# Performance work log

Hardware: AMD Instinct MI355X
Metric: run time of the kernel (lower is better)

## Reference

```python
import jax, jax.numpy as jnp
import numpy as np

N_NODES = 50000
IN_FEATS, HID_FEATS, OUT_FEATS, HEADS = 128, 32, 64, 4
NEG_SLOPE = 0.2
EPS = 1e-16


def gat_conv(x, src, dst, W, att_src, att_dst, bias, heads, out_ch, concat):
    """PyG-style GATConv. src/dst: [E] (self-loops already included).
    W: [in, heads*out_ch]; att_src/att_dst: [heads, out_ch]; bias: [heads*out_ch] or [out_ch].
    """
    n = x.shape[0]
    xw = (x @ W).reshape(n, heads, out_ch)                     # [N,H,C]
    a_src = (xw * att_src).sum(-1)                             # [N,H]
    a_dst = (xw * att_dst).sum(-1)                             # [N,H]
    e = jax.nn.leaky_relu(a_src[src] + a_dst[dst], NEG_SLOPE)  # [E,H]
    # segment softmax over incoming edges of each destination node
    m = jax.ops.segment_max(e, dst, num_segments=n)
    e = jnp.exp(e - m[dst])
    denom = jax.ops.segment_sum(e, dst, num_segments=n)
    alpha = e / (denom[dst] + EPS)                             # [E,H]
    out = jax.ops.segment_sum(alpha[:, :, None] * xw[src], dst, num_segments=n)  # [N,H,C]
    out = out.reshape(n, heads * out_ch) if concat else out.mean(axis=1)
    return out + bias


def setup_inputs() -> dict:
    key = jax.random.key(0)
    ks = jax.random.split(key, 10)
    E = 1600000
    x = jax.random.normal(ks[0], (N_NODES, IN_FEATS), dtype=jnp.float32)
    edge_index = jax.random.randint(ks[1], (2, E), 0, N_NODES, dtype=jnp.int64)
    s1 = 1.0 / np.sqrt(IN_FEATS)
    W1 = jax.random.uniform(ks[2], (IN_FEATS, HEADS * HID_FEATS), jnp.float32, -s1, s1)
    att_src1 = jax.random.normal(ks[3], (HEADS, HID_FEATS), dtype=jnp.float32) * 0.1
    att_dst1 = jax.random.normal(ks[4], (HEADS, HID_FEATS), dtype=jnp.float32) * 0.1
    b1 = jnp.zeros((HEADS * HID_FEATS,), jnp.float32)
    s2 = 1.0 / np.sqrt(HEADS * HID_FEATS)
    W2 = jax.random.uniform(ks[5], (HEADS * HID_FEATS, OUT_FEATS), jnp.float32, -s2, s2)
    att_src2 = jax.random.normal(ks[6], (1, OUT_FEATS), dtype=jnp.float32) * 0.1
    att_dst2 = jax.random.normal(ks[7], (1, OUT_FEATS), dtype=jnp.float32) * 0.1
    b2 = jnp.zeros((OUT_FEATS,), jnp.float32)
    return {"x": x, "edge_index": edge_index, "W1": W1, "att_src1": att_src1,
            "att_dst1": att_dst1, "b1": b1, "W2": W2, "att_src2": att_src2,
            "att_dst2": att_dst2, "b2": b2}


def reference(x, edge_index, W1, att_src1, att_dst1, b1, W2, att_src2, att_dst2, b2):
    n = x.shape[0]
    loops = jnp.arange(n, dtype=edge_index.dtype)
    src = jnp.concatenate([edge_index[0], loops])
    dst = jnp.concatenate([edge_index[1], loops])
    h = gat_conv(x, src, dst, W1, att_src1, att_dst1, b1, HEADS, HID_FEATS, True)
    h = jax.nn.elu(h)
    h = gat_conv(h, src, dst, W2, att_src2, att_dst2, b2, 1, OUT_FEATS, False)
    return h.mean(axis=0)
```

## Files before the change

### kernel.cpp

```cpp
#include <hip/hip_runtime.h>
#include <math.h>

#define N_NODES 50000
#define SN      N_NODES
#define E_RAW   1600000
#define TE      (E_RAW + N_NODES)
#define TEP     (TE + 16 * N_NODES)
#define F_IN    128
#define H1      4
#define F1      128
#define F2      64
#define NEG_SLOPE 0.2f
#define EPS_F   1e-16f
#define XPAD    136

#define NBINS   196
#define NBLK_A  128
#define EPB     ((TE + NBLK_A - 1) / NBLK_A)
#define MM_BLOCKS (N_NODES / 16)

__device__ __forceinline__ float lrelu(float v) { return v > 0.f ? v : NEG_SLOPE * v; }

typedef float vf2 __attribute__((ext_vector_type(2)));
typedef short short8 __attribute__((ext_vector_type(8)));
typedef float f32x4 __attribute__((ext_vector_type(4)));

__device__ __forceinline__ unsigned short f2bf(float f) {
    unsigned u = __float_as_uint(f);
    return (unsigned short)((u + 0x7fffu + ((u >> 16) & 1u)) >> 16);
}
__device__ __forceinline__ unsigned char f2fp8(float f) {
    int p = __builtin_amdgcn_cvt_pk_fp8_f32(f, f, 0, false);
    return (unsigned char)(p & 0xff);
}
__device__ __forceinline__ vf2 fp8lo(unsigned u) {
    return __builtin_amdgcn_cvt_pk_f32_fp8((int)u, false);
}
__device__ __forceinline__ vf2 fp8hi(unsigned u) {
    return __builtin_amdgcn_cvt_pk_f32_fp8((int)u, true);
}

__global__ __launch_bounds__(256) void k_prep(const float* __restrict__ W1,
                                              const float* __restrict__ W2,
                                              unsigned short* __restrict__ w1t,
                                              unsigned short* __restrict__ w2t,
                                              float* __restrict__ a1s,
                                              float* __restrict__ a2s) {
    int idx = blockIdx.x * 256 + threadIdx.x;
    if (idx < 16384) {
        int c = idx >> 7, k = idx & 127;
        w1t[idx] = f2bf(W1[k * F1 + c]);
    } else {
        int j = idx - 16384;
        int c = j >> 7, k = j & 127;
        w2t[j] = f2bf(W2[k * F2 + c]);
    }
    if (blockIdx.x == 0 && threadIdx.x < H1) a1s[SN * H1 + threadIdx.x] = -1e30f;
    if (blockIdx.x == 0 && threadIdx.x == H1) a2s[SN] = -1e30f;
}

__global__ __launch_bounds__(256) void k_l1_mm_hist(
    const float* __restrict__ x, const unsigned short* __restrict__ w1t,
    const float* __restrict__ atts, const float* __restrict__ attd,
    unsigned char* __restrict__ xwf8, float* __restrict__ a1s, float* __restrict__ a1d,
    const int* __restrict__ ei, int* __restrict__ cnt) {
    __shared__ __align__(16) unsigned short wls[F1 * XPAD];
    __shared__ __align__(16) unsigned short xs[16 * XPAD];
    const int t = threadIdx.x;
    if (blockIdx.x >= MM_BLOCKS) {
        int* hist = (int*)wls;
        const int blk = blockIdx.x - MM_BLOCKS;
        for (int i = t; i < NBINS; i += 256) hist[i] = 0;
        __syncthreads();
        const int e0 = blk * EPB, e1 = min(TE, e0 + EPB);
        for (int e = e0 + t; e < e1; e += 256) {
            int d = (e < E_RAW) ? ei[E_RAW + e] : (e - E_RAW);
            atomicAdd(&hist[d >> 8], 1);
        }
        __syncthreads();
        for (int i = t; i < NBINS; i += 256) cnt[i * NBLK_A + blk] = hist[i];
        return;
    }
    const int n0 = blockIdx.x * 16;
    {
        const float4* src = (const float4*)(x + (size_t)n0 * F_IN);
#pragma unroll
        for (int i = 0; i < 2; ++i) {
            int idx = t + 256 * i;
            float4 v = src[idx];
            int row = idx >> 5;
            int col = (idx & 31) * 4;
            ushort4 o = { f2bf(v.x), f2bf(v.y), f2bf(v.z), f2bf(v.w) };
            *(ushort4*)(xs + row * XPAD + col) = o;
        }
        const uint4* wsrc = (const uint4*)w1t;
#pragma unroll
        for (int i = 0; i < 8; ++i) {
            int idx = t + 256 * i;
            uint4 v = wsrc[idx];
            int row = idx >> 4;
            int col = (idx & 15) * 8;
            *(uint4*)(wls + row * XPAD + col) = v;
        }
    }
    __syncthreads();
    const int w = t >> 6;
    const int lane = t & 63;
    const int quad = lane >> 4;
    const int ncol = lane & 15;
    const int ch0 = w * 32;
    const unsigned short* arow = xs + ncol * XPAD;
    const unsigned short* brow0 = wls + (ch0 + ncol) * XPAD;
    const unsigned short* brow1 = brow0 + 16 * XPAD;
    f32x4 acc0 = {0.f, 0.f, 0.f, 0.f}, acc1 = {0.f, 0.f, 0.f, 0.f};
#pragma unroll
    for (int s = 0; s < 4; ++s) {
        int kb = s * 32 + quad * 8;
        short8 a  = *(const short8*)(arow + kb);
        short8 b0 = *(const short8*)(brow0 + kb);
        short8 b1 = *(const short8*)(brow1 + kb);
        acc0 = __builtin_amdgcn_mfma_f32_16x16x32_bf16(a, b0, acc0, 0, 0, 0);
        acc1 = __builtin_amdgcn_mfma_f32_16x16x32_bf16(a, b1, acc1, 0, 0, 0);
    }
    const int ch = ch0 + ncol;
    const float as0 = atts[ch], as1 = atts[ch + 16];
    const float ad0 = attd[ch], ad1 = attd[ch + 16];
#pragma unroll
    for (int reg = 0; reg < 4; ++reg) {
        const int n = n0 + quad * 4 + reg;
        float v0 = acc0[reg], v1 = acc1[reg];
        xwf8[(size_t)n * F1 + ch] = f2fp8(v0);
        xwf8[(size_t)n * F1 + ch + 16] = f2fp8(v1);
        float ps = fmaf(v0, as0, v1 * as1);
        float pd = fmaf(v0, ad0, v1 * ad1);
#pragma unroll
        for (int off = 1; off < 16; off <<= 1) {
            ps += __shfl_xor(ps, off);
            pd += __shfl_xor(pd, off);
        }
        if (ncol == 0) {
            a1s[n * H1 + w] = ps;
            a1d[n * H1 + w] = pd;
        }
    }
}

__global__ __launch_bounds__(64) void k_btot(int* __restrict__ cnt, int* __restrict__ btot) {
    const int bin = blockIdx.x, lane = threadIdx.x;
    int c0 = cnt[bin * NBLK_A + 2 * lane];
    int c1 = cnt[bin * NBLK_A + 2 * lane + 1];
    int s = c0 + c1;
    int incl = s;
#pragma unroll
    for (int off = 1; off < 64; off <<= 1) {
        int u = __shfl_up(incl, off, 64);
        if (lane >= off) incl += u;
    }
    int excl = incl - s;
    cnt[bin * NBLK_A + 2 * lane] = excl;
    cnt[bin * NBLK_A + 2 * lane + 1] = excl + c0;
    if (lane == 63) btot[bin] = incl;
}

__global__ __launch_bounds__(64) void k_bstart(const int* __restrict__ btot,
                                               int* __restrict__ bstart) {
    const int lane = threadIdx.x;
    int v[4]; int s = 0;
#pragma unroll
    for (int j = 0; j < 4; ++j) {
        int i = 4 * lane + j;
        v[j] = (i < NBINS) ? btot[i] : 0;
        s += v[j];
    }
    int incl = s;
#pragma unroll
    for (int off = 1; off < 64; off <<= 1) {
        int u = __shfl_up(incl, off, 64);
        if (lane >= off) incl += u;
    }
    int run = incl - s;
#pragma unroll
    for (int j = 0; j < 4; ++j) {
        int i = 4 * lane + j;
        if (i < NBINS) bstart[i] = run;
        run += v[j];
    }
    if (lane == 63) bstart[NBINS] = TE;
}

__global__ __launch_bounds__(256) void k_scatter_coarse(const int* __restrict__ ei,
                                                        const int* __restrict__ cnt,
                                                        const int* __restrict__ bstart,
                                                        unsigned* __restrict__ cbuf) {
    __shared__ int cur[NBINS];
    const int t = threadIdx.x, blk = blockIdx.x;
    for (int i = t; i < NBINS; i += 256) cur[i] = cnt[i * NBLK_A + blk] + bstart[i];
    __syncthreads();
    const int e0 = blk * EPB, e1 = min(TE, e0 + EPB);
    for (int e = e0 + t; e < e1; e += 256) {
        int s, d;
        if (e < E_RAW) { s = ei[e]; d = ei[E_RAW + e]; }
        else { s = e - E_RAW; d = s; }
        int pos = atomicAdd(&cur[d >> 8], 1);
        cbuf[pos] = ((unsigned)(d & 255) << 16) | (unsigned)s;
    }
}

__global__ __launch_bounds__(256) void k_fine_hist(const unsigned* __restrict__ cbuf,
                                                   const int* __restrict__ bstart,
                                                   int* __restrict__ deg) {
    __shared__ int hist[256];
    const int t = threadIdx.x, b = blockIdx.x;
    hist[t] = 0;
    __syncthreads();
    const int i0 = bstart[b], i1 = bstart[b + 1];
    for (int i = i0 + t; i < i1; i += 256) atomicAdd(&hist[cbuf[i] >> 16], 1);
    __syncthreads();
    const int d = b * 256 + t;
    if (d < N_NODES) deg[d] = hist[t];
}

__global__ __launch_bounds__(1024) void k_scan1(const int* __restrict__ deg,
                                                int* __restrict__ incl, int* __restrict__ bsum) {
    int t = threadIdx.x, g = blockIdx.x;
    int idx = g * 1024 + t;
    int v = (idx < N_NODES) ? ((deg[idx] + 15) & ~15) : 0;
    int lane = t & 63, w = t >> 6;
#pragma unroll
    for (int off = 1; off < 64; off <<= 1) {
        int u = __shfl_up(v, off, 64);
        if (lane >= off) v += u;
    }
    __shared__ int ws[16];
    if (lane == 63) ws[w] = v;
    __syncthreads();
    if (w == 0 && lane < 16) {
        int s = ws[lane];
#pragma unroll
        for (int off = 1; off < 16; off <<= 1) {
            int u = __shfl_up(s, off, 16);
            if (lane >= off) s += u;
        }
        ws[lane] = s;
    }
    __syncthreads();
    if (w > 0) v += ws[w - 1];
    if (idx < N_NODES) incl[idx] = v;
    if (t == 1023) bsum[g] = v;
}

__global__ void k_scan2(int* __restrict__ bsum, int nblk) {
    int t = threadIdx.x;
    int v = (t < nblk) ? bsum[t] : 0;
#pragma unroll
    for (int off = 1; off < 64; off <<= 1) {
        int u = __shfl_up(v, off, 64);
        if (t >= off) v += u;
    }
    if (t < nblk) bsum[t] = v;
}

__global__ __launch_bounds__(1024) void k_scan3(const int* __restrict__ incl,
                                                const int* __restrict__ bsum,
                                                int* __restrict__ rowstart) {
    int idx = blockIdx.x * 1024 + threadIdx.x;
    if (idx >= N_NODES) return;
    int off = (blockIdx.x > 0) ? bsum[blockIdx.x - 1] : 0;
    rowstart[idx + 1] = incl[idx] + off;
    if (idx == 0) rowstart[0] = 0;
}

__global__ __launch_bounds__(256) void k_build_csr(const unsigned* __restrict__ cbuf,
                                                   const int* __restrict__ bstart,
                                                   const int* __restrict__ rowstart,
                                                   const int* __restrict__ deg,
                                                   int* __restrict__ csr) {
    __shared__ int cur[256];
    const int t = threadIdx.x, b = blockIdx.x;
    const int d = b * 256 + t;
    cur[t] = (d < N_NODES) ? rowstart[d] : 0;
    __syncthreads();
    const int i0 = bstart[b], i1 = bstart[b + 1];
    for (int i = i0 + t; i < i1; i += 256) {
        unsigned v = cbuf[i];
        int pos = atomicAdd(&cur[v >> 16], 1);
        csr[pos] = (int)(v & 0xffffu);
    }
    __syncthreads();
    if (d < N_NODES) {
        const int pend = rowstart[d] + ((deg[d] + 15) & ~15);
        for (int i = cur[t]; i < pend; ++i) csr[i] = SN;
    }
}

__global__ __launch_bounds__(256) void k_l1_gather(
    const int* __restrict__ rowstart, const int* __restrict__ csr,
    const int* __restrict__ deg, const float* __restrict__ a1s,
    const float* __restrict__ a1d, const unsigned* __restrict__ xwu,
    const float* __restrict__ b1, float* __restrict__ h1) {
    const int lane = threadIdx.x & 63;
    const int wid = threadIdx.x >> 6;
    const int n = blockIdx.x * 4 + wid;
    if (n >= N_NODES) return;
    const int rs = rowstart[n];
    const int nb16 = (deg[n] + 15) >> 4;
    const int half = lane >> 5;
    const int sub = lane & 31;
    const int h = sub >> 3;
    const float adh = a1d[n * H1 + h];
    const int4* c4 = (const int4*)(csr + rs);
    const int eoff = half * 8 + (sub & 7);
    const int wbase = half * 32 + (h << 3);
    float den = 0.f, f0 = 0.f, f1 = 0.f, f2 = 0.f, f3 = 0.f;
    for (int b = 0; b < nb16; ++b) {
        const int i0 = 4 * b + 2 * half;
        int4 sA = c4[i0], sB = c4[i0 + 1];
        int se = csr[rs + 16 * b + eoff];
        unsigned u0 = xwu[sA.x * 32 + sub], u1 = xwu[sA.y * 32 + sub];
        unsigned u2 = xwu[sA.z * 32 + sub], u3 = xwu[sA.w * 32 + sub];
        unsigned u4 = xwu[sB.x * 32 + sub], u5 = xwu[sB.y * 32 + sub];
        unsigned u6 = xwu[sB.z * 32 + sub], u7 = xwu[sB.w * 32 + sub];
        float we = __expf(lrelu(a1s[se * H1 + h] + adh));
        float w0 = __shfl(we, wbase + 0), w1 = __shfl(we, wbase + 1);
        float w2 = __shfl(we, wbase + 2), w3 = __shfl(we, wbase + 3);
        float w4 = __shfl(we, wbase + 4), w5 = __shfl(we, wbase + 5);
        float w6 = __shfl(we, wbase + 6), w7 = __shfl(we, wbase + 7);
        den += ((w0 + w1) + (w2 + w3)) + ((w4 + w5) + (w6 + w7));
        vf2 l0 = fp8lo(u0), v0 = fp8hi(u0);
        f0 = fmaf(w0, l0.x, f0); f1 = fmaf(w0, l0.y, f1);
        f2 = fmaf(w0, v0.x, f2); f3 = fmaf(w0, v0.y, f3);
        vf2 l1 = fp8lo(u1), v1 = fp8hi(u1);
        f0 = fmaf(w1, l1.x, f0); f1 = fmaf(w1, l1.y, f1);
        f2 = fmaf(w1, v1.x, f2); f3 = fmaf(w1, v1.y, f3);
        vf2 l2 = fp8lo(u2), v2 = fp8hi(u2);
        f0 = fmaf(w2, l2.x, f0); f1 = fmaf(w2, l2.y, f1);
        f2 = fmaf(w2, v2.x, f2); f3 = fmaf(w2, v2.y, f3);
        vf2 l3 = fp8lo(u3), v3 = fp8hi(u3);
        f0 = fmaf(w3, l3.x, f0); f1 = fmaf(w3, l3.y, f1);
        f2 = fmaf(w3, v3.x, f2); f3 = fmaf(w3, v3.y, f3);
        vf2 l4 = fp8lo(u4), v4 = fp8hi(u4);
        f0 = fmaf(w4, l4.x, f0); f1 = fmaf(w4, l4.y, f1);
        f2 = fmaf(w4, v4.x, f2); f3 = fmaf(w4, v4.y, f3);
        vf2 l5 = fp8lo(u5), v5 = fp8hi(u5);
        f0 = fmaf(w5, l5.x, f0); f1 = fmaf(w5, l5.y, f1);
        f2 = fmaf(w5, v5.x, f2); f3 = fmaf(w5, v5.y, f3);
        vf2 l6 = fp8lo(u6), v6 = fp8hi(u6);
        f0 = fmaf(w6, l6.x, f0); f1 = fmaf(w6, l6.y, f1);
        f2 = fmaf(w6, v6.x, f2); f3 = fmaf(w6, v6.y, f3);
        vf2 l7 = fp8lo(u7), v7 = fp8hi(u7);
        f0 = fmaf(w7, l7.x, f0); f1 = fmaf(w7, l7.y, f1);
        f2 = fmaf(w7, v7.x, f2); f3 = fmaf(w7, v7.y, f3);
    }
    f0 += __shfl_xor(f0, 32);
    f1 += __shfl_xor(f1, 32);
    f2 += __shfl_xor(f2, 32);
    f3 += __shfl_xor(f3, 32);
    den += __shfl_xor(den, 32);
    if (half == 0) {
        const float inv = 1.f / (den + EPS_F);
        float4 bb = ((const float4*)b1)[sub];
        float o0 = fmaf(f0, inv, bb.x);
        float o1 = fmaf(f1, inv, bb.y);
        float o2 = fmaf(f2, inv, bb.z);
        float o3 = fmaf(f3, inv, bb.w);
        o0 = o0 > 0.f ? o0 : expm1f(o0);
        o1 = o1 > 0.f ? o1 : expm1f(o1);
        o2 = o2 > 0.f ? o2 : expm1f(o2);
        o3 = o3 > 0.f ? o3 : expm1f(o3);
        ((float4*)h1)[(size_t)n * 32 + sub] = make_float4(o0, o1, o2, o3);
    }
}

__global__ __launch_bounds__(256) void k_l2_mm(
    const float* __restrict__ h1, const unsigned short* __restrict__ w2t,
    const float* __restrict__ atts, const float* __restrict__ attd,
    unsigned char* __restrict__ xwf8, float* __restrict__ a2s, float* __restrict__ a2d) {
    __shared__ __align__(16) unsigned short wls[F2 * XPAD];
    __shared__ __align__(16) unsigned short xs[16 * XPAD];
    __shared__ float parts[16][4], partd[16][4];
    const int t = threadIdx.x;
    const int n0 = blockIdx.x * 16;
    {
        const float4* src = (const float4*)(h1 + (size_t)n0 * F1);
#pragma unroll
        for (int i = 0; i < 2; ++i) {
            int idx = t + 256 * i;
            float4 v = src[idx];
            int row = idx >> 5;
            int col = (idx & 31) * 4;
            ushort4 o = { f2bf(v.x), f2bf(v.y), f2bf(v.z), f2bf(v.w) };
            *(ushort4*)(xs + row * XPAD + col) = o;
        }
        const uint4* wsrc = (const uint4*)w2t;
#pragma unroll
        for (int i = 0; i < 4; ++i) {
            int idx = t + 256 * i;
            uint4 v = wsrc[idx];
            int row = idx >> 4;
            int col = (idx & 15) * 8;
            *(uint4*)(wls + row * XPAD + col) = v;
        }
    }
    __syncthreads();
    const int w = t >> 6;
    const int lane = t & 63;
    const int quad = lane >> 4;
    const int ncol = lane & 15;
    const int ch0 = w * 16;
    const unsigned short* arow = xs + ncol * XPAD;
    const unsigned short* brow = wls + (ch0 + ncol) * XPAD;
    f32x4 acc = {0.f, 0.f, 0.f, 0.f};
#pragma unroll
    for (int s = 0; s < 4; ++s) {
        int kb = s * 32 + quad * 8;
        short8 a = *(const short8*)(arow + kb);
        short8 b = *(const short8*)(brow + kb);
        acc = __builtin_amdgcn_mfma_f32_16x16x32_bf16(a, b, acc, 0, 0, 0);
    }
    const int ch = ch0 + ncol;
    const float asv = atts[ch], adv = attd[ch];
#pragma unroll
    for (int reg = 0; reg < 4; ++reg) {
        const int m = quad * 4 + reg;
        float v = acc[reg];
        xwf8[(size_t)(n0 + m) * F2 + ch] = f2fp8(v);
        float ps = v * asv, pd = v * adv;
#pragma unroll
        for (int off = 1; off < 16; off <<= 1) {
            ps += __shfl_xor(ps, off);
            pd += __shfl_xor(pd, off);
        }
        if (ncol == 0) { parts[m][w] = ps; partd[m][w] = pd; }
    }
    __syncthreads();
    if (t < 16) {
        a2s[n0 + t] = (parts[t][0] + parts[t][1]) + (parts[t][2] + parts[t][3]);
        a2d[n0 + t] = (partd[t][0] + partd[t][1]) + (partd[t][2] + partd[t][3]);
    }
}

__global__ __launch_bounds__(256) void k_l2_gather(
    const int* __restrict__ rowstart, const int* __restrict__ csr,
    const int* __restrict__ deg, const float* __restrict__ a2s,
    const float* __restrict__ a2d, const unsigned* __restrict__ xwu,
    float* __restrict__ h2) {
    const int lane = threadIdx.x & 63;
    const int wid = threadIdx.x >> 6;
    const int n = blockIdx.x * 4 + wid;
    if (n >= N_NODES) return;
    const int rs = rowstart[n];
    const int nb16 = (deg[n] + 15) >> 4;
    const int q = lane >> 4;
    const int sub = lane & 15;
    const float adv = a2d[n];
    const int4* c4 = (const int4*)(csr + rs);
    float den = 0.f, f0 = 0.f, f1 = 0.f, f2 = 0.f, f3 = 0.f;
    for (int b = 0; b < nb16; ++b) {
        int4 s4 = c4[4 * b + q];
        int se = csr[rs + 16 * b + sub];
        unsigned u0 = xwu[s4.x * 16 + sub], u1 = xwu[s4.y * 16 + sub];
        unsigned u2 = xwu[s4.z * 16 + sub], u3 = xwu[s4.w * 16 + sub];
        float we = __expf(lrelu(a2s[se] + adv));
        float w0 = __shfl(we, 4 * q + 0), w1 = __shfl(we, 4 * q + 1);
        float w2 = __shfl(we, 4 * q + 2), w3 = __shfl(we, 4 * q + 3);
        den += (w0 + w1) + (w2 + w3);
        vf2 l0 = fp8lo(u0), v0 = fp8hi(u0);
        f0 = fmaf(w0, l0.x, f0); f1 = fmaf(w0, l0.y, f1);
        f2 = fmaf(w0, v0.x, f2); f3 = fmaf(w0, v0.y, f3);
        vf2 l1 = fp8lo(u1), v1 = fp8hi(u1);
        f0 = fmaf(w1, l1.x, f0); f1 = fmaf(w1, l1.y, f1);
        f2 = fmaf(w1, v1.x, f2); f3 = fmaf(w1, v1.y, f3);
        vf2 l2 = fp8lo(u2), v2 = fp8hi(u2);
        f0 = fmaf(w2, l2.x, f0); f1 = fmaf(w2, l2.y, f1);
        f2 = fmaf(w2, v2.x, f2); f3 = fmaf(w2, v2.y, f3);
        vf2 l3 = fp8lo(u3), v3 = fp8hi(u3);
        f0 = fmaf(w3, l3.x, f0); f1 = fmaf(w3, l3.y, f1);
        f2 = fmaf(w3, v3.x, f2); f3 = fmaf(w3, v3.y, f3);
    }
#pragma unroll
    for (int off = 16; off <= 32; off <<= 1) {
        f0 += __shfl_xor(f0, off);
        f1 += __shfl_xor(f1, off);
        f2 += __shfl_xor(f2, off);
        f3 += __shfl_xor(f3, off);
        den += __shfl_xor(den, off);
    }
    if (lane < 16) {
        const float inv = 1.f / (den + EPS_F);
        ((float4*)h2)[(size_t)n * 16 + sub] =
            make_float4(f0 * inv, f1 * inv, f2 * inv, f3 * inv);
    }
}

#define MEAN_BLOCKS 256
__global__ __launch_bounds__(256) void k_mean(const float* __restrict__ h2,
                                              double* __restrict__ accum) {
    const int t = threadIdx.x;
    const int c = t & 63;
    double acc = 0.0;
    const size_t total = (size_t)N_NODES * F2;
    for (size_t idx = (size_t)blockIdx.x * 256 + t; idx < total; idx += (size_t)MEAN_BLOCKS * 256)
        acc += (double)h2[idx];
    __shared__ double red[256];
    red[t] = acc;
    __syncthreads();
    if (t < 64) {
        double v = red[t] + red[t + 64] + red[t + 128] + red[t + 192];
        atomicAdd(&accum[c], v);
    }
}

__global__ void k_final(const double* __restrict__ accum, const float* __restrict__ b2,
                        float* __restrict__ out) {
    int t = threadIdx.x;
    if (t < F2) out[t] = (float)(accum[t] * (1.0 / (double)N_NODES)) + b2[t];
}

extern "C" void kernel_launch(void* const* d_in, const int* in_sizes, int n_in,
                              void* d_out, int out_size, void* d_ws, size_t ws_size,
                              hipStream_t stream) {
    (void)in_sizes; (void)n_in; (void)out_size; (void)ws_size;
    const float* x   = (const float*)d_in[0];
    const int*   ei  = (const int*)d_in[1];
    const float* W1  = (const float*)d_in[2];
    const float* as1 = (const float*)d_in[3];
    const float* ad1 = (const float*)d_in[4];
    const float* b1  = (const float*)d_in[5];
    const float* W2  = (const float*)d_in[6];
    const float* as2 = (const float*)d_in[7];
    const float* ad2 = (const float*)d_in[8];
    const float* b2  = (const float*)d_in[9];
    float* out = (float*)d_out;

    char* ws = (char*)d_ws;
    size_t off = 0;
    auto alloc = [&](size_t bytes) -> void* {
        void* p = ws + off;
        off += (bytes + 255) & ~(size_t)255;
        return p;
    };
    unsigned char*  xw1f8 = (unsigned char*)alloc((size_t)(N_NODES + 1) * F1);
    float* h1       = (float*)alloc((size_t)N_NODES * F1 * 4);
    unsigned char*  xw2f8 = (unsigned char*)alloc((size_t)(N_NODES + 1) * F2);
    float* h2       = (float*)alloc((size_t)N_NODES * F2 * 4);
    unsigned short* w1t = (unsigned short*)alloc((size_t)F1 * F1 * 2);
    unsigned short* w2t = (unsigned short*)alloc((size_t)F2 * F1 * 2);
    float* a1s      = (float*)alloc((size_t)(N_NODES + 1) * H1 * 4);
    float* a1d      = (float*)alloc((size_t)N_NODES * H1 * 4);
    float* a2s      = (float*)alloc((size_t)(N_NODES + 1) * 4);
    float* a2d      = (float*)alloc((size_t)N_NODES * 4);
    int*   deg      = (int*)alloc((size_t)N_NODES * 4);
    unsigned* cbuf  = (unsigned*)alloc((size_t)TE * 4);
    int*   cnt      = (int*)alloc((size_t)NBINS * NBLK_A * 4);
    int*   btot     = (int*)alloc((size_t)NBINS * 4);
    int*   bstart   = (int*)alloc((size_t)(NBINS + 1) * 4);
    int*   rowstart = (int*)alloc((size_t)(N_NODES + 1) * 4);
    int*   csr      = (int*)alloc((size_t)TEP * 4);
    int*   incl     = (int*)alloc((size_t)N_NODES * 4);
    int*   bsum     = (int*)alloc(64 * 4);
    double* accum   = (double*)alloc(F2 * 8);

    const int nscan = (N_NODES + 1023) / 1024;
    const int nwave4 = (N_NODES + 3) / 4;

    hipMemsetAsync(accum, 0, F2 * 8, stream);
    k_prep<<<96, 256, 0, stream>>>(W1, W2, w1t, w2t, a1s, a2s);
    k_l1_mm_hist<<<MM_BLOCKS + NBLK_A, 256, 0, stream>>>(x, w1t, as1, ad1, xw1f8, a1s, a1d, ei, cnt);
    k_btot<<<NBINS, 64, 0, stream>>>(cnt, btot);
    k_bstart<<<1, 64, 0, stream>>>(btot, bstart);
    k_scatter_coarse<<<NBLK_A, 256, 0, stream>>>(ei, cnt, bstart, cbuf);
    k_fine_hist<<<NBINS, 256, 0, stream>>>(cbuf, bstart, deg);
    k_scan1<<<nscan, 1024, 0, stream>>>(deg, incl, bsum);
    k_scan2<<<1, 64, 0, stream>>>(bsum, nscan);
    k_scan3<<<nscan, 1024, 0, stream>>>(incl, bsum, rowstart);
    k_build_csr<<<NBINS, 256, 0, stream>>>(cbuf, bstart, rowstart, deg, csr);
    k_l1_gather<<<nwave4, 256, 0, stream>>>(rowstart, csr, deg, a1s, a1d,
                                            (const unsigned*)xw1f8, b1, h1);
    k_l2_mm<<<MM_BLOCKS, 256, 0, stream>>>(h1, w2t, as2, ad2, xw2f8, a2s, a2d);
    k_l2_gather<<<nwave4, 256, 0, stream>>>(rowstart, csr, deg, a2s, a2d,
                                            (const unsigned*)xw2f8, h2);
    k_mean<<<MEAN_BLOCKS, 256, 0, stream>>>(h2, accum);
    k_final<<<1, 64, 0, stream>>>(accum, b2, out);
}
```

Measured before the change: 268.3 us.

## Merge small scan kernels, fold final into mean, prefetch CSR and use exp2 in gathers

Merges the bin-total and bin-start kernels into one single-block kernel, drops the second scan pass by having each scan3 block reduce the preceding block sums itself, and folds the final output kernel into k_mean through a last-block counter. These cut the number of small serial launches. The gather kernels prefetch the next CSR indices and attention scores, replace expf with exp2 by prescaling the attention vectors by log2(e), use packed FMA, and accumulate the denominator per lane. The extra zero row for padding edges is now initialised explicitly. The last-block pattern relies on fences and atomics to be correct.

```diff
diff --git a/kernel.cpp b/kernel.cpp
--- a/kernel.cpp
+++ b/kernel.cpp
@@ -13,14 +13,13 @@
 #define NEG_SLOPE 0.2f
 #define EPS_F   1e-16f
 #define XPAD    136
+#define LOG2E   1.4426950408889634f
 
 #define NBINS   196
 #define NBLK_A  128
 #define EPB     ((TE + NBLK_A - 1) / NBLK_A)
 #define MM_BLOCKS (N_NODES / 16)
 
-__device__ __forceinline__ float lrelu(float v) { return v > 0.f ? v : NEG_SLOPE * v; }
-
 typedef float vf2 __attribute__((ext_vector_type(2)));
 typedef short short8 __attribute__((ext_vector_type(8)));
 typedef float f32x4 __attribute__((ext_vector_type(4)));
@@ -38,6 +37,23 @@
 }
 __device__ __forceinline__ vf2 fp8hi(unsigned u) {
     return __builtin_amdgcn_cvt_pk_f32_fp8((int)u, true);
+}
+__device__ __forceinline__ vf2 pkfma(float w, vf2 a, vf2 c) {
+#if __has_builtin(__builtin_elementwise_fma)
+    vf2 wv = {w, w};
+    return __builtin_elementwise_fma(wv, a, c);
+#else
+    c.x = fmaf(w, a.x, c.x);
+    c.y = fmaf(w, a.y, c.y);
+    return c;
+#endif
+}
+__device__ __forceinline__ float fexp2(float x) {
+#if __has_builtin(__builtin_amdgcn_exp2f)
+    return __builtin_amdgcn_exp2f(x);
+#else
+    return exp2f(x);
+#endif
 }
 
 __global__ __launch_bounds__(256) void k_prep(const float* __restrict__ W1,
@@ -45,7 +61,9 @@
                                               unsigned short* __restrict__ w1t,
                                               unsigned short* __restrict__ w2t,
                                               float* __restrict__ a1s,
-                                              float* __restrict__ a2s) {
+                                              float* __restrict__ a2s,
+                                              unsigned* __restrict__ xw1row,
+                                              unsigned* __restrict__ xw2row) {
     int idx = blockIdx.x * 256 + threadIdx.x;
     if (idx < 16384) {
         int c = idx >> 7, k = idx & 127;
@@ -57,6 +75,10 @@
     }
     if (blockIdx.x == 0 && threadIdx.x < H1) a1s[SN * H1 + threadIdx.x] = -1e30f;
     if (blockIdx.x == 0 && threadIdx.x == H1) a2s[SN] = -1e30f;
+    if (blockIdx.x == 1) {
+        if (threadIdx.x < 32) xw1row[threadIdx.x] = 0u;
+        else if (threadIdx.x < 48) xw2row[threadIdx.x - 32] = 0u;
+    }
 }
 
 __global__ __launch_bounds__(256) void k_l1_mm_hist(
@@ -123,8 +145,8 @@
         acc1 = __builtin_amdgcn_mfma_f32_16x16x32_bf16(a, b1, acc1, 0, 0, 0);
     }
     const int ch = ch0 + ncol;
-    const float as0 = atts[ch], as1 = atts[ch + 16];
-    const float ad0 = attd[ch], ad1 = attd[ch + 16];
+    const float as0 = atts[ch] * LOG2E, as1 = atts[ch + 16] * LOG2E;
+    const float ad0 = attd[ch] * LOG2E, ad1 = attd[ch + 16] * LOG2E;
 #pragma unroll
     for (int reg = 0; reg < 4; ++reg) {
         const int n = n0 + quad * 4 + reg;
@@ -145,47 +167,49 @@
     }
 }
 
-__global__ __launch_bounds__(64) void k_btot(int* __restrict__ cnt, int* __restrict__ btot) {
-    const int bin = blockIdx.x, lane = threadIdx.x;
-    int c0 = cnt[bin * NBLK_A + 2 * lane];
-    int c1 = cnt[bin * NBLK_A + 2 * lane + 1];
-    int s = c0 + c1;
-    int incl = s;
-#pragma unroll
-    for (int off = 1; off < 64; off <<= 1) {
-        int u = __shfl_up(incl, off, 64);
-        if (lane >= off) incl += u;
-    }
-    int excl = incl - s;
-    cnt[bin * NBLK_A + 2 * lane] = excl;
-    cnt[bin * NBLK_A + 2 * lane + 1] = excl + c0;
-    if (lane == 63) btot[bin] = incl;
-}
-
-__global__ __launch_bounds__(64) void k_bstart(const int* __restrict__ btot,
-                                               int* __restrict__ bstart) {
-    const int lane = threadIdx.x;
-    int v[4]; int s = 0;
-#pragma unroll
-    for (int j = 0; j < 4; ++j) {
-        int i = 4 * lane + j;
-        v[j] = (i < NBINS) ? btot[i] : 0;
-        s += v[j];
-    }
-    int incl = s;
-#pragma unroll
-    for (int off = 1; off < 64; off <<= 1) {
-        int u = __shfl_up(incl, off, 64);
-        if (lane >= off) incl += u;
-    }
-    int run = incl - s;
-#pragma unroll
-    for (int j = 0; j < 4; ++j) {
-        int i = 4 * lane + j;
-        if (i < NBINS) bstart[i] = run;
-        run += v[j];
-    }
-    if (lane == 63) bstart[NBINS] = TE;
+__global__ __launch_bounds__(1024) void k_binscan(int* __restrict__ cnt,
+                                                  int* __restrict__ bstart) {
+    __shared__ int bt[NBINS];
+    const int t = threadIdx.x, lane = t & 63, w = t >> 6;
+    for (int bin = w; bin < NBINS; bin += 16) {
+        int c0 = cnt[bin * NBLK_A + 2 * lane];
+        int c1 = cnt[bin * NBLK_A + 2 * lane + 1];
+        int s = c0 + c1;
+        int incl = s;
+#pragma unroll
+        for (int off = 1; off < 64; off <<= 1) {
+            int u = __shfl_up(incl, off, 64);
+            if (lane >= off) incl += u;
+        }
+        int excl = incl - s;
+        cnt[bin * NBLK_A + 2 * lane] = excl;
+        cnt[bin * NBLK_A + 2 * lane + 1] = excl + c0;
+        if (lane == 63) bt[bin] = incl;
+    }
+    __syncthreads();
+    if (w == 0) {
+        int v[4]; int s = 0;
+#pragma unroll
+        for (int j = 0; j < 4; ++j) {
+            int i = 4 * lane + j;
+            v[j] = (i < NBINS) ? bt[i] : 0;
+            s += v[j];
+        }
+        int incl = s;
+#pragma unroll
+        for (int off = 1; off < 64; off <<= 1) {
+            int u = __shfl_up(incl, off, 64);
+            if (lane >= off) incl += u;
+        }
+        int run = incl - s;
+#pragma unroll
+        for (int j = 0; j < 4; ++j) {
+            int i = 4 * lane + j;
+            if (i < NBINS) bstart[i] = run;
+            run += v[j];
+        }
+        if (lane == 63) bstart[NBINS] = TE;
+    }
 }
 
 __global__ __launch_bounds__(256) void k_scatter_coarse(const int* __restrict__ ei,
@@ -249,24 +273,20 @@
     if (t == 1023) bsum[g] = v;
 }
 
-__global__ void k_scan2(int* __restrict__ bsum, int nblk) {
-    int t = threadIdx.x;
-    int v = (t < nblk) ? bsum[t] : 0;
-#pragma unroll
-    for (int off = 1; off < 64; off <<= 1) {
-        int u = __shfl_up(v, off, 64);
-        if (t >= off) v += u;
-    }
-    if (t < nblk) bsum[t] = v;
-}
-
 __global__ __launch_bounds__(1024) void k_scan3(const int* __restrict__ incl,
                                                 const int* __restrict__ bsum,
                                                 int* __restrict__ rowstart) {
-    int idx = blockIdx.x * 1024 + threadIdx.x;
-    if (idx >= N_NODES) return;
-    int off = (blockIdx.x > 0) ? bsum[blockIdx.x - 1] : 0;
-    rowstart[idx + 1] = incl[idx] + off;
+    __shared__ int soff;
+    const int t = threadIdx.x;
+    if (t < 64) {
+        int v = (t < blockIdx.x) ? bsum[t] : 0;
+#pragma unroll
+        for (int off = 32; off >= 1; off >>= 1) v += __shfl_xor(v, off, 64);
+        if (t == 0) soff = v;
+    }
+    __syncthreads();
+    const int idx = blockIdx.x * 1024 + t;
+    if (idx < N_NODES) rowstart[idx + 1] = incl[idx] + soff;
     if (idx == 0) rowstart[0] = 0;
 }
 
@@ -309,59 +329,61 @@
     const int h = sub >> 3;
     const float adh = a1d[n * H1 + h];
     const int4* c4 = (const int4*)(csr + rs);
-    const int eoff = half * 8 + (sub & 7);
     const int wbase = half * 32 + (h << 3);
-    float den = 0.f, f0 = 0.f, f1 = 0.f, f2 = 0.f, f3 = 0.f;
+    const bool s1 = (sub & 1) != 0, s2 = (sub & 2) != 0, s4b = (sub & 4) != 0;
+    vf2 f01 = {0.f, 0.f}, f23 = {0.f, 0.f};
+    float den_l = 0.f;
+    int4 sA = c4[2 * half], sB = c4[2 * half + 1];
+    int se = s4b ? (s2 ? (s1 ? sB.w : sB.z) : (s1 ? sB.y : sB.x))
+                 : (s2 ? (s1 ? sA.w : sA.z) : (s1 ? sA.y : sA.x));
+    float asv = a1s[se * H1 + h];
     for (int b = 0; b < nb16; ++b) {
-        const int i0 = 4 * b + 2 * half;
-        int4 sA = c4[i0], sB = c4[i0 + 1];
-        int se = csr[rs + 16 * b + eoff];
+        int4 nA, nB;
+        if (b + 1 < nb16) {
+            nA = c4[4 * (b + 1) + 2 * half];
+            nB = c4[4 * (b + 1) + 2 * half + 1];
+        }
         unsigned u0 = xwu[sA.x * 32 + sub], u1 = xwu[sA.y * 32 + sub];
         unsigned u2 = xwu[sA.z * 32 + sub], u3 = xwu[sA.w * 32 + sub];
         unsigned u4 = xwu[sB.x * 32 + sub], u5 = xwu[sB.y * 32 + sub];
         unsigned u6 = xwu[sB.z * 32 + sub], u7 = xwu[sB.w * 32 + sub];
-        float we = __expf(lrelu(a1s[se * H1 + h] + adh));
+        float sv = asv + adh;
+        float we = fexp2(fmaxf(sv, NEG_SLOPE * sv));
+        den_l += we;
         float w0 = __shfl(we, wbase + 0), w1 = __shfl(we, wbase + 1);
         float w2 = __shfl(we, wbase + 2), w3 = __shfl(we, wbase + 3);
         float w4 = __shfl(we, wbase + 4), w5 = __shfl(we, wbase + 5);
         float w6 = __shfl(we, wbase + 6), w7 = __shfl(we, wbase + 7);
-        den += ((w0 + w1) + (w2 + w3)) + ((w4 + w5) + (w6 + w7));
-        vf2 l0 = fp8lo(u0), v0 = fp8hi(u0);
-        f0 = fmaf(w0, l0.x, f0); f1 = fmaf(w0, l0.y, f1);
-        f2 = fmaf(w0, v0.x, f2); f3 = fmaf(w0, v0.y, f3);
-        vf2 l1 = fp8lo(u1), v1 = fp8hi(u1);
-        f0 = fmaf(w1, l1.x, f0); f1 = fmaf(w1, l1.y, f1);
-        f2 = fmaf(w1, v1.x, f2); f3 = fmaf(w1, v1.y, f3);
-        vf2 l2 = fp8lo(u2), v2 = fp8hi(u2);
-        f0 = fmaf(w2, l2.x, f0); f1 = fmaf(w2, l2.y, f1);
-        f2 = fmaf(w2, v2.x, f2); f3 = fmaf(w2, v2.y, f3);
-        vf2 l3 = fp8lo(u3), v3 = fp8hi(u3);
-        f0 = fmaf(w3, l3.x, f0); f1 = fmaf(w3, l3.y, f1);
-        f2 = fmaf(w3, v3.x, f2); f3 = fmaf(w3, v3.y, f3);
-        vf2 l4 = fp8lo(u4), v4 = fp8hi(u4);
-        f0 = fmaf(w4, l4.x, f0); f1 = fmaf(w4, l4.y, f1);
-        f2 = fmaf(w4, v4.x, f2); f3 = fmaf(w4, v4.y, f3);
-        vf2 l5 = fp8lo(u5), v5 = fp8hi(u5);
-        f0 = fmaf(w5, l5.x, f0); f1 = fmaf(w5, l5.y, f1);
-        f2 = fmaf(w5, v5.x, f2); f3 = fmaf(w5, v5.y, f3);
-        vf2 l6 = fp8lo(u6), v6 = fp8hi(u6);
-        f0 = fmaf(w6, l6.x, f0); f1 = fmaf(w6, l6.y, f1);
-        f2 = fmaf(w6, v6.x, f2); f3 = fmaf(w6, v6.y, f3);
-        vf2 l7 = fp8lo(u7), v7 = fp8hi(u7);
-        f0 = fmaf(w7, l7.x, f0); f1 = fmaf(w7, l7.y, f1);
-        f2 = fmaf(w7, v7.x, f2); f3 = fmaf(w7, v7.y, f3);
-    }
+        f01 = pkfma(w0, fp8lo(u0), f01); f23 = pkfma(w0, fp8hi(u0), f23);
+        f01 = pkfma(w1, fp8lo(u1), f01); f23 = pkfma(w1, fp8hi(u1), f23);
+        f01 = pkfma(w2, fp8lo(u2), f01); f23 = pkfma(w2, fp8hi(u2), f23);
+        f01 = pkfma(w3, fp8lo(u3), f01); f23 = pkfma(w3, fp8hi(u3), f23);
+        f01 = pkfma(w4, fp8lo(u4), f01); f23 = pkfma(w4, fp8hi(u4), f23);
+        f01 = pkfma(w5, fp8lo(u5), f01); f23 = pkfma(w5, fp8hi(u5), f23);
+        f01 = pkfma(w6, fp8lo(u6), f01); f23 = pkfma(w6, fp8hi(u6), f23);
+        f01 = pkfma(w7, fp8lo(u7), f01); f23 = pkfma(w7, fp8hi(u7), f23);
+        if (b + 1 < nb16) {
+            se = s4b ? (s2 ? (s1 ? nB.w : nB.z) : (s1 ? nB.y : nB.x))
+                     : (s2 ? (s1 ? nA.w : nA.z) : (s1 ? nA.y : nA.x));
+            asv = a1s[se * H1 + h];
+            sA = nA; sB = nB;
+        }
+    }
+    float f0 = f01.x, f1 = f01.y, f2v = f23.x, f3 = f23.y;
     f0 += __shfl_xor(f0, 32);
     f1 += __shfl_xor(f1, 32);
-    f2 += __shfl_xor(f2, 32);
+    f2v += __shfl_xor(f2v, 32);
     f3 += __shfl_xor(f3, 32);
-    den += __shfl_xor(den, 32);
+    den_l += __shfl_xor(den_l, 1);
+    den_l += __shfl_xor(den_l, 2);
+    den_l += __shfl_xor(den_l, 4);
+    den_l += __shfl_xor(den_l, 32);
     if (half == 0) {
-        const float inv = 1.f / (den + EPS_F);
+        const float inv = 1.f / (den_l + EPS_F);
         float4 bb = ((const float4*)b1)[sub];
         float o0 = fmaf(f0, inv, bb.x);
         float o1 = fmaf(f1, inv, bb.y);
-        float o2 = fmaf(f2, inv, bb.z);
+        float o2 = fmaf(f2v, inv, bb.z);
         float o3 = fmaf(f3, inv, bb.w);
         o0 = o0 > 0.f ? o0 : expm1f(o0);
         o1 = o1 > 0.f ? o1 : expm1f(o1);
@@ -418,7 +440,7 @@
         acc = __builtin_amdgcn_mfma_f32_16x16x32_bf16(a, b, acc, 0, 0, 0);
     }
     const int ch = ch0 + ncol;
-    const float asv = atts[ch], adv = attd[ch];
+    const float asv = atts[ch] * LOG2E, adv = attd[ch] * LOG2E;
 #pragma unroll
     for (int reg = 0; reg < 4; ++reg) {
         const int m = quad * 4 + reg;
@@ -454,47 +476,56 @@
     const int sub = lane & 15;
     const float adv = a2d[n];
     const int4* c4 = (const int4*)(csr + rs);
-    float den = 0.f, f0 = 0.f, f1 = 0.f, f2 = 0.f, f3 = 0.f;
+    const int wsrc = 16 * q;
+    const bool s1 = (sub & 1) != 0, s2 = (sub & 2) != 0;
+    vf2 f01 = {0.f, 0.f}, f23 = {0.f, 0.f};
+    float den_l = 0.f;
+    int4 sA = c4[q];
+    int se = s2 ? (s1 ? sA.w : sA.z) : (s1 ? sA.y : sA.x);
+    float asv = a2s[se];
     for (int b = 0; b < nb16; ++b) {
-        int4 s4 = c4[4 * b + q];
-        int se = csr[rs + 16 * b + sub];
-        unsigned u0 = xwu[s4.x * 16 + sub], u1 = xwu[s4.y * 16 + sub];
-        unsigned u2 = xwu[s4.z * 16 + sub], u3 = xwu[s4.w * 16 + sub];
-        float we = __expf(lrelu(a2s[se] + adv));
-        float w0 = __shfl(we, 4 * q + 0), w1 = __shfl(we, 4 * q + 1);
-        float w2 = __shfl(we, 4 * q + 2), w3 = __shfl(we, 4 * q + 3);
-        den += (w0 + w1) + (w2 + w3);
-        vf2 l0 = fp8lo(u0), v0 = fp8hi(u0);
-        f0 = fmaf(w0, l0.x, f0); f1 = fmaf(w0, l0.y, f1);
-        f2 = fmaf(w0, v0.x, f2); f3 = fmaf(w0, v0.y, f3);
-        vf2 l1 = fp8lo(u1), v1 = fp8hi(u1);
-        f0 = fmaf(w1, l1.x, f0); f1 = fmaf(w1, l1.y, f1);
-        f2 = fmaf(w1, v1.x, f2); f3 = fmaf(w1, v1.y, f3);
-        vf2 l2 = fp8lo(u2), v2 = fp8hi(u2);
-        f0 = fmaf(w2, l2.x, f0); f1 = fmaf(w2, l2.y, f1);
-        f2 = fmaf(w2, v2.x, f2); f3 = fmaf(w2, v2.y, f3);
-        vf2 l3 = fp8lo(u3), v3 = fp8hi(u3);
-        f0 = fmaf(w3, l3.x, f0); f1 = fmaf(w3, l3.y, f1);
-        f2 = fmaf(w3, v3.x, f2); f3 = fmaf(w3, v3.y, f3);
-    }
+        int4 nA;
+        if (b + 1 < nb16) nA = c4[4 * (b + 1) + q];
+        unsigned u0 = xwu[sA.x * 16 + sub], u1 = xwu[sA.y * 16 + sub];
+        unsigned u2 = xwu[sA.z * 16 + sub], u3 = xwu[sA.w * 16 + sub];
+        float sv = asv + adv;
+        float we = fexp2(fmaxf(sv, NEG_SLOPE * sv));
+        den_l += we;
+        float w0 = __shfl(we, wsrc + 0), w1 = __shfl(we, wsrc + 1);
+        float w2 = __shfl(we, wsrc + 2), w3 = __shfl(we, wsrc + 3);
+        f01 = pkfma(w0, fp8lo(u0), f01); f23 = pkfma(w0, fp8hi(u0), f23);
+        f01 = pkfma(w1, fp8lo(u1), f01); f23 = pkfma(w1, fp8hi(u1), f23);
+        f01 = pkfma(w2, fp8lo(u2), f01); f23 = pkfma(w2, fp8hi(u2), f23);
+        f01 = pkfma(w3, fp8lo(u3), f01); f23 = pkfma(w3, fp8hi(u3), f23);
+        if (b + 1 < nb16) {
+            se = s2 ? (s1 ? nA.w : nA.z) : (s1 ? nA.y : nA.x);
+            asv = a2s[se];
+            sA = nA;
+        }
+    }
+    float f0 = f01.x, f1 = f01.y, f2v = f23.x, f3 = f23.y;
 #pragma unroll
     for (int off = 16; off <= 32; off <<= 1) {
         f0 += __shfl_xor(f0, off);
         f1 += __shfl_xor(f1, off);
-        f2 += __shfl_xor(f2, off);
+        f2v += __shfl_xor(f2v, off);
         f3 += __shfl_xor(f3, off);
-        den += __shfl_xor(den, off);
-    }
+    }
+#pragma unroll
+    for (int off = 1; off <= 32; off <<= 1) den_l += __shfl_xor(den_l, off);
     if (lane < 16) {
-        const float inv = 1.f / (den + EPS_F);
+        const float inv = 1.f / (0.25f * den_l + EPS_F);
         ((float4*)h2)[(size_t)n * 16 + sub] =
-            make_float4(f0 * inv, f1 * inv, f2 * inv, f3 * inv);
+            make_float4(f0 * inv, f1 * inv, f2v * inv, f3 * inv);
     }
 }
 
 #define MEAN_BLOCKS 256
 __global__ __launch_bounds__(256) void k_mean(const float* __restrict__ h2,
-                                              double* __restrict__ accum) {
+                                              double* __restrict__ accum,
+                                              const float* __restrict__ b2,
+                                              float* __restrict__ out,
+                                              unsigned* __restrict__ ctr) {
     const int t = threadIdx.x;
     const int c = t & 63;
     double acc = 0.0;
@@ -502,18 +533,27 @@
     for (size_t idx = (size_t)blockIdx.x * 256 + t; idx < total; idx += (size_t)MEAN_BLOCKS * 256)
         acc += (double)h2[idx];
     __shared__ double red[256];
+    __shared__ int lastflag;
     red[t] = acc;
     __syncthreads();
     if (t < 64) {
         double v = red[t] + red[t + 64] + red[t + 128] + red[t + 192];
         atomicAdd(&accum[c], v);
     }
-}
-
-__global__ void k_final(const double* __restrict__ accum, const float* __restrict__ b2,
-                        float* __restrict__ out) {
-    int t = threadIdx.x;
-    if (t < F2) out[t] = (float)(accum[t] * (1.0 / (double)N_NODES)) + b2[t];
+    __threadfence();
+    __syncthreads();
+    if (t == 0) {
+        unsigned done = atomicAdd(ctr, 1u);
+        lastflag = (done == MEAN_BLOCKS - 1) ? 1 : 0;
+    }
+    __syncthreads();
+    if (lastflag) {
+        __threadfence();
+        if (t < F2) {
+            double v = atomicAdd(&accum[t], 0.0);
+            out[t] = (float)(v * (1.0 / (double)N_NODES)) + b2[t];
+        }
+    }
 }
 
 extern "C" void kernel_launch(void* const* d_in, const int* in_sizes, int n_in,
@@ -552,26 +592,26 @@
     int*   deg      = (int*)alloc((size_t)N_NODES * 4);
     unsigned* cbuf  = (unsigned*)alloc((size_t)TE * 4);
     int*   cnt      = (int*)alloc((size_t)NBINS * NBLK_A * 4);
-    int*   btot     = (int*)alloc((size_t)NBINS * 4);
     int*   bstart   = (int*)alloc((size_t)(NBINS + 1) * 4);
     int*   rowstart = (int*)alloc((size_t)(N_NODES + 1) * 4);
     int*   csr      = (int*)alloc((size_t)TEP * 4);
     int*   incl     = (int*)alloc((size_t)N_NODES * 4);
     int*   bsum     = (int*)alloc(64 * 4);
-    double* accum   = (double*)alloc(F2 * 8);
+    double* accum   = (double*)alloc(F2 * 8 + 16);
+    unsigned* ctr   = (unsigned*)(accum + F2);
 
     const int nscan = (N_NODES + 1023) / 1024;
     const int nwave4 = (N_NODES + 3) / 4;
 
-    hipMemsetAsync(accum, 0, F2 * 8, stream);
-    k_prep<<<96, 256, 0, stream>>>(W1, W2, w1t, w2t, a1s, a2s);
+    hipMemsetAsync(accum, 0, F2 * 8 + 16, stream);
+    k_prep<<<96, 256, 0, stream>>>(W1, W2, w1t, w2t, a1s, a2s,
+                                   (unsigned*)(xw1f8 + (size_t)SN * F1),
+                                   (unsigned*)(xw2f8 + (size_t)SN * F2));
     k_l1_mm_hist<<<MM_BLOCKS + NBLK_A, 256, 0, stream>>>(x, w1t, as1, ad1, xw1f8, a1s, a1d, ei, cnt);
-    k_btot<<<NBINS, 64, 0, stream>>>(cnt, btot);
-    k_bstart<<<1, 64, 0, stream>>>(btot, bstart);
+    k_binscan<<<1, 1024, 0, stream>>>(cnt, bstart);
     k_scatter_coarse<<<NBLK_A, 256, 0, stream>>>(ei, cnt, bstart, cbuf);
     k_fine_hist<<<NBINS, 256, 0, stream>>>(cbuf, bstart, deg);
     k_scan1<<<nscan, 1024, 0, stream>>>(deg, incl, bsum);
-    k_scan2<<<1, 64, 0, stream>>>(bsum, nscan);
     k_scan3<<<nscan, 1024, 0, stream>>>(incl, bsum, rowstart);
     k_build_csr<<<NBINS, 256, 0, stream>>>(cbuf, bstart, rowstart, deg, csr);
     k_l1_gather<<<nwave4, 256, 0, stream>>>(rowstart, csr, deg, a1s, a1d,
@@ -579,6 +619,5 @@
     k_l2_mm<<<MM_BLOCKS, 256, 0, stream>>>(h1, w2t, as2, ad2, xw2f8, a2s, a2d);
     k_l2_gather<<<nwave4, 256, 0, stream>>>(rowstart, csr, deg, a2s, a2d,
                                             (const unsigned*)xw2f8, h2);
-    k_mean<<<MEAN_BLOCKS, 256, 0, stream>>>(h2, accum);
-    k_final<<<1, 64, 0, stream>>>(accum, b2, out);
-}
+    k_mean<<<MEAN_BLOCKS, 256, 0, stream>>>(h2, accum, b2, out, ctr);
+}
```

Result: slower. 282.8 us (+5.4%).
